# Performance work log

Measured on AMD Instinct MI355X. Metric: run time of the kernel, lower is better.

## Reference

```python
import jax, jax.numpy as jnp
import numpy as np
from jax import lax

# Dimensions (must match input_specs)
B, T, C = 2, 2048, 1024
H = 4 * C          # FFN hidden
E_RWKV, E_TRANS = 6, 2
E = E_RWKV + E_TRANS
LN_EPS = 1e-5


def layernorm(x, g, b):
    m = x.mean(-1, keepdims=True)
    v = ((x - m) ** 2).mean(-1, keepdims=True)
    return (x - m) * lax.rsqrt(v + LN_EPS) * g + b


def setup_inputs() -> dict:
    key = jax.random.key(0)
    ks = jax.random.split(key, 24)
    s = 0.02
    inp = {
        "x": jax.random.normal(ks[0], (B, T, C), jnp.float32),
        "v_first": jax.random.normal(ks[1], (B, T, C), jnp.float32),
        "winners": jax.random.randint(ks[2], (B, T, 2), 0, E),
        "capital_shares": jax.random.uniform(ks[3], (E,), jnp.float32),
        # LayerNorms
        "ln1_g": jnp.ones((C,), jnp.float32), "ln1_b": jnp.zeros((C,), jnp.float32),
        "ln2_g": jnp.ones((C,), jnp.float32), "ln2_b": jnp.zeros((C,), jnp.float32),
        # RWKV-style time-mix (simplified RWKV7_TimeMix)
        "Wr": s * jax.random.normal(ks[4], (C, C), jnp.float32),
        "Wk": s * jax.random.normal(ks[5], (C, C), jnp.float32),
        "Wv": s * jax.random.normal(ks[6], (C, C), jnp.float32),
        "Wo": s * jax.random.normal(ks[7], (C, C), jnp.float32),
        "w_decay": jax.random.normal(ks[8], (C,), jnp.float32),
        "g_v": jax.random.normal(ks[9], (C,), jnp.float32),
        # bridge: linear on concat(h, rwkv_state)
        "Wb": s * jax.random.normal(ks[10], (2 * C, C), jnp.float32),
        "bb": jnp.zeros((C,), jnp.float32),
        # 6 stacked SparseRWKVFFN experts: sigmoid(x Wr_r) * (relu(x Wk_r)^2 Wv_r)
        "Wk_r": s * jax.random.normal(ks[11], (E_RWKV, C, H), jnp.float32),
        "Wv_r": s * jax.random.normal(ks[12], (E_RWKV, H, C), jnp.float32),
        "Wr_r": s * jax.random.normal(ks[13], (E_RWKV, C, C), jnp.float32),
        # 2 stacked LinearTransformerExpert: gelu((h+prefix) W1) W2
        "W1_t": s * jax.random.normal(ks[14], (E_TRANS, C, H), jnp.float32),
        "W2_t": s * jax.random.normal(ks[15], (E_TRANS, H, C), jnp.float32),
    }
    return inp


def reference(x, v_first, winners, capital_shares,
              ln1_g, ln1_b, ln2_g, ln2_b,
              Wr, Wk, Wv, Wo, w_decay, g_v,
              Wb, bb, Wk_r, Wv_r, Wr_r, W1_t, W2_t):
    # ---- attention (simplified RWKV time-mix), returns per-token state ----
    h1 = layernorm(x, ln1_g, ln1_b)
    r = jax.nn.sigmoid(h1 @ Wr)                      # [B,T,C]
    k = h1 @ Wk
    v = h1 @ Wv
    v = v + (v_first - v) * jax.nn.sigmoid(g_v)      # value-residual mix
    w = jax.nn.sigmoid(w_decay)                      # per-channel decay [C]

    def step(s, kv):
        k_t, v_t = kv                                # [B,C] each
        s = w * s + k_t * v_t
        return s, s

    s0 = jnp.zeros((B, C), x.dtype)
    _, states = lax.scan(step, s0, (jnp.swapaxes(k, 0, 1), jnp.swapaxes(v, 0, 1)))
    states = jnp.swapaxes(states, 0, 1)              # rwkv_state [B,T,C]

    att_out = (r * states) @ Wo
    x = x + att_out
    h = layernorm(x, ln2_g, ln2_b)

    # ---- bridge prefix (flat over tokens, vectorized) ----
    bridge_prefix = jnp.concatenate([h, states], axis=-1) @ Wb + bb  # [B,T,C]

    # ---- experts computed densely, combined by top-2 gates ----
    # RWKV FFN experts
    a = jnp.square(jax.nn.relu(jnp.einsum('btc,ech->ebth', h, Wk_r)))     # [Er,B,T,H]
    rec = jax.nn.sigmoid(jnp.einsum('btc,ecd->ebtd', h, Wr_r))            # [Er,B,T,C]
    out_r = rec * jnp.einsum('ebth,ehc->ebtc', a, Wv_r)                   # [Er,B,T,C]
    # Linear-transformer experts consume the bridge prefix
    ht = h + bridge_prefix
    out_t = jnp.einsum('ebth,ehc->ebtc',
                       jax.nn.gelu(jnp.einsum('btc,ech->ebth', ht, W1_t)),
                       W2_t)                                              # [Et,B,T,C]
    all_out = jnp.concatenate([out_r, out_t], axis=0)                     # [E,B,T,C]

    # top-2 combine, each rank weighted 0.5 (use_market=False branch)
    gate = 0.5 * (jax.nn.one_hot(winners[..., 0], E, dtype=x.dtype)
                  + jax.nn.one_hot(winners[..., 1], E, dtype=x.dtype))    # [B,T,E]
    final_out = jnp.einsum('ebtc,bte->btc', all_out, gate)

    return x + final_out
```

## Files before the change

### kernel.cpp

```cpp
#include <hip/hip_runtime.h>

typedef unsigned short u16;
typedef __bf16 bf16x8 __attribute__((ext_vector_type(8)));
typedef float f32x4 __attribute__((ext_vector_type(4)));

__device__ __forceinline__ float bf2f(u16 u){ union{unsigned i;float f;}x; x.i=((unsigned)u)<<16; return x.f; }
__device__ __forceinline__ u16 f2bf(float f){ union{float f;unsigned i;}x; x.f=f; unsigned r = x.i + 0x7FFFu + ((x.i>>16)&1u); return (u16)(r>>16); }
__device__ __forceinline__ float sigm(float x){ return 1.f/(1.f+expf(-x)); }

struct __align__(8) U16x4 { u16 v[4]; };

__global__ void conv_t(const float* __restrict__ src, u16* __restrict__ dst, int K, int N){
  __shared__ u16 tile[64][72];
  const size_t mo = (size_t)blockIdx.z * (size_t)K * (size_t)N;
  src += mo; dst += mo;
  int k0 = blockIdx.x*64, n0 = blockIdx.y*64;
  int tid = threadIdx.x;
  #pragma unroll
  for (int it=0; it<4; ++it){
    int e = it*1024 + tid*4;
    int r = e>>6, c = e&63;
    float4 v = *(const float4*)(src + (size_t)(k0+r)*N + n0 + c);
    tile[r][c+0]=f2bf(v.x); tile[r][c+1]=f2bf(v.y); tile[r][c+2]=f2bf(v.z); tile[r][c+3]=f2bf(v.w);
  }
  __syncthreads();
  #pragma unroll
  for (int it=0; it<4; ++it){
    int e = it*1024 + tid*4;
    int n = e>>6, k = e&63;
    U16x4 o;
    #pragma unroll
    for (int j=0;j<4;++j) o.v[j] = tile[k+j][n];
    *(U16x4*)(dst + (size_t)(n0+n)*K + k0 + k) = o;
  }
}

__global__ void ln_k(const float* __restrict__ x, const float* __restrict__ g, const float* __restrict__ b,
                     u16* __restrict__ out, int ostride){
  int row = blockIdx.x, tid = threadIdx.x;
  float4 v = *(const float4*)(x + (size_t)row*1024 + tid*4);
  float s = v.x+v.y+v.z+v.w;
  float ss = v.x*v.x+v.y*v.y+v.z*v.z+v.w*v.w;
  #pragma unroll
  for (int o=32;o;o>>=1){ s += __shfl_down(s,o); ss += __shfl_down(ss,o); }
  __shared__ float sm[8];
  int lane = tid&63, wv = tid>>6;
  if (!lane){ sm[wv]=s; sm[4+wv]=ss; }
  __syncthreads();
  s = sm[0]+sm[1]+sm[2]+sm[3]; ss = sm[4]+sm[5]+sm[6]+sm[7];
  float mean = s*(1.f/1024.f);
  float var = ss*(1.f/1024.f) - mean*mean;
  float inv = rsqrtf(var + 1e-5f);
  U16x4 o;
  const float* vp = &v.x;
  #pragma unroll
  for (int j=0;j<4;++j){
    int c = tid*4+j;
    o.v[j] = f2bf((vp[j]-mean)*inv*g[c] + b[c]);
  }
  *(U16x4*)(out + (size_t)row*ostride + tid*4) = o;
}

__global__ void scan_p1(const u16* __restrict__ kbuf, const u16* __restrict__ vbuf,
                        const float* __restrict__ w_decay, float* __restrict__ carry){
  int c = blockIdx.x*256 + threadIdx.x;
  int chunk = blockIdx.y, b = blockIdx.z;
  float w = sigm(w_decay[c]);
  float s = 0.f;
  size_t idx = ((size_t)(b*2048 + chunk*64))*1024 + c;
  #pragma unroll 4
  for (int i=0;i<64;++i){ s = w*s + bf2f(kbuf[idx])*bf2f(vbuf[idx]); idx += 1024; }
  carry[((size_t)(b*32+chunk))*1024 + c] = s;
}
__global__ void scan_p2(const float* __restrict__ w_decay, const float* __restrict__ carry,
                        float* __restrict__ startv){
  int c = blockIdx.x*256 + threadIdx.x;
  int b = blockIdx.y;
  float w = sigm(w_decay[c]);
  float wL = w;
  #pragma unroll
  for (int i=0;i<6;++i) wL *= wL;
  float p = 0.f;
  for (int j=0;j<32;++j){
    size_t id = ((size_t)(b*32+j))*1024 + c;
    startv[id] = p;
    p = wL*p + carry[id];
  }
}
__global__ void scan_p3(const u16* __restrict__ kbuf, const u16* __restrict__ vbuf, const u16* __restrict__ rbuf,
                        const float* __restrict__ w_decay, const float* __restrict__ startv,
                        u16* __restrict__ rs, u16* __restrict__ hcat){
  int c = blockIdx.x*256 + threadIdx.x;
  int chunk = blockIdx.y, b = blockIdx.z;
  float w = sigm(w_decay[c]);
  float s = startv[((size_t)(b*32+chunk))*1024 + c];
  size_t t0 = (size_t)b*2048 + chunk*64;
  size_t idx = t0*1024 + c;
  size_t idx2 = t0*2048 + 1024 + c;
  for (int i=0;i<64;++i){
    s = w*s + bf2f(kbuf[idx])*bf2f(vbuf[idx]);
    rs[idx] = f2bf(bf2f(rbuf[idx]) * s);
    hcat[idx2] = f2bf(s);
    idx += 1024; idx2 += 2048;
  }
}

__global__ void route_count(const int* __restrict__ winners, int* __restrict__ offs, int* __restrict__ cursor){
  __shared__ int cnt[8];
  if (threadIdx.x < 8) cnt[threadIdx.x] = 0;
  __syncthreads();
  for (int p = threadIdx.x; p < 8192; p += 256) atomicAdd(&cnt[winners[p]&7], 1);
  __syncthreads();
  if (threadIdx.x == 0){
    int s = 0;
    #pragma unroll
    for (int e=0;e<8;++e){ offs[e]=s; s+=cnt[e]; }
    offs[8]=s;
  }
  if (threadIdx.x < 8) cursor[threadIdx.x] = 0;
}
__global__ void route_scatter(const int* __restrict__ winners, const int* __restrict__ offs,
                              int* __restrict__ cursor, int* __restrict__ idx_all){
  int p = blockIdx.x*256 + threadIdx.x;
  if (p < 8192){
    int e = winners[p]&7;
    int pos = offs[e] + atomicAdd(&cursor[e], 1);
    idx_all[pos] = p>>1;
  }
}

struct GArgs {
  const u16* A; const u16* B;
  long long lda, bstride;
  int K, N, Mdense, eBase;
  const int* offs; const int* idx_all;
  const float* x; const float* v_first; const float* g_v;
  u16* rbuf; u16* kbuf; u16* vbuf;
  float* out;
  const u16* hcat; const float* bb; u16* ht;
  u16* act; u16* rec;
};

template<int EPI, int GATHER>
__global__ __launch_bounds__(256,2) void gemm_k(GArgs g){
  int e = g.eBase + blockIdx.z;
  int rbase = 0, m = g.Mdense;
  if (g.offs){ rbase = g.offs[e]; m = g.offs[e+1] - rbase; }
  if ((int)blockIdx.y * 128 >= m) return;
  __shared__ char smem[32768];
  const int tid = threadIdx.x, lane = tid&63, wave = tid>>6;
  const int wr = wave>>1, wc = wave&1;

  int srow[4], scol[4];
  #pragma unroll
  for (int i=0;i<4;++i){
    srow[i] = i*32 + (tid>>3);
    scol[i] = ((((tid&7)*16) ^ ((srow[i]&7)<<4)) >> 1);
  }
  const u16* bBase[4];
  #pragma unroll
  for (int i=0;i<4;++i)
    bBase[i] = g.B + (long long)blockIdx.z*g.bstride
             + ((long long)blockIdx.x*128 + srow[i])*(long long)g.K + scol[i];

  int aOff[4][2], bOff[4][2];
  #pragma unroll
  for (int mm=0;mm<4;++mm){
    int rm = wr*64 + mm*16 + (lane&15);
    int rn = wc*64 + mm*16 + (lane&15);
    #pragma unroll
    for (int kk=0;kk<2;++kk){
      int X = kk*64 + (lane>>4)*16;
      aOff[mm][kk] = rm*128 + (X ^ ((rm&7)<<4));
      bOff[mm][kk] = 16384 + rn*128 + (X ^ ((rn&7)<<4));
    }
  }
  char* ldsA = smem + wave*1024;
  char* ldsB = smem + 16384 + wave*1024;
  const int nk = g.K >> 6;

  for (int mt = blockIdx.y; mt*128 < m; mt += gridDim.y){
    const u16* aSrc[4]; const u16* bSrc[4];
    #pragma unroll
    for (int i=0;i<4;++i){
      int grow = mt*128 + srow[i];
      int lr = grow < m ? grow : m-1;
      long long arow;
      if (GATHER) arow = g.idx_all[rbase + lr];
      else if (g.offs) arow = rbase + lr;
      else arow = grow;
      aSrc[i] = g.A + arow*g.lda + scol[i];
      bSrc[i] = bBase[i];
    }
    f32x4 acc[4][4];
    #pragma unroll
    for (int mm=0;mm<4;++mm)
      #pragma unroll
      for (int nn=0;nn<4;++nn)
        acc[mm][nn] = f32x4{0.f,0.f,0.f,0.f};

    for (int ks=0; ks<nk; ++ks){
      #pragma unroll
      for (int i=0;i<4;++i){
        __builtin_amdgcn_global_load_lds((const __attribute__((address_space(1))) void*)aSrc[i],
                                         (__attribute__((address_space(3))) void*)(ldsA + i*4096), 16, 0, 0);
        __builtin_amdgcn_global_load_lds((const __attribute__((address_space(1))) void*)bSrc[i],
                                         (__attribute__((address_space(3))) void*)(ldsB + i*4096), 16, 0, 0);
        aSrc[i] += 64; bSrc[i] += 64;
      }
      __syncthreads();
      #pragma unroll
      for (int kk=0;kk<2;++kk){
        bf16x8 af[4], bfv[4];
        #pragma unroll
        for (int q=0;q<4;++q) af[q] = *(const bf16x8*)(smem + aOff[q][kk]);
        #pragma unroll
        for (int q=0;q<4;++q) bfv[q] = *(const bf16x8*)(smem + bOff[q][kk]);
        #pragma unroll
        for (int mm=0;mm<4;++mm)
          #pragma unroll
          for (int nn=0;nn<4;++nn)
            acc[mm][nn] = __builtin_amdgcn_mfma_f32_16x16x32_bf16(af[mm], bfv[nn], acc[mm][nn], 0,0,0);
      }
      __syncthreads();
    }

    int colBase = blockIdx.x*128 + wc*64 + (lane&15);
    #pragma unroll
    for (int mm=0;mm<4;++mm){
      #pragma unroll
      for (int j=0;j<4;++j){
        int grow = mt*128 + wr*64 + mm*16 + (lane>>4)*4 + j;
        if (grow >= m) continue;
        size_t t = (size_t)grow;
        int gr = rbase + grow;
        #pragma unroll
        for (int nn=0;nn<4;++nn){
          int col = colBase + nn*16;
          float val = acc[mm][nn][j];
          if (EPI==0){
            if (col < 1024) g.rbuf[t*1024+col] = f2bf(sigm(val));
            else if (col < 2048) g.kbuf[t*1024+col-1024] = f2bf(val);
            else {
              int c2 = col-2048;
              float sg = sigm(g.g_v[c2]);
              float vf = g.v_first[t*1024+c2];
              g.vbuf[t*1024+c2] = f2bf(val + (vf-val)*sg);
            }
          } else if (EPI==1){
            g.out[t*1024+col] = g.x[t*1024+col] + val;
          } else if (EPI==2){
            g.ht[t*1024+col] = f2bf(bf2f(g.hcat[t*2048+col]) + val + g.bb[col]);
          } else if (EPI==3){
            float r_ = fmaxf(val, 0.f);
            g.act[(size_t)gr*4096+col] = f2bf(r_*r_);
          } else if (EPI==4){
            g.rec[(size_t)gr*1024+col] = f2bf(sigm(val));
          } else if (EPI==5){
            int tok = g.idx_all[gr];
            float rc = bf2f(g.rec[(size_t)gr*1024+col]);
            atomicAdd(&g.out[(size_t)tok*1024+col], 0.5f*val*rc);
          } else if (EPI==6){
            float t3 = val*val*val;
            float th = tanhf(0.79788456080286535588f*(val + 0.044715f*t3));
            g.act[(size_t)gr*4096+col] = f2bf(0.5f*val*(1.f+th));
          } else if (EPI==7){
            int tok = g.idx_all[gr];
            atomicAdd(&g.out[(size_t)tok*1024+col], 0.5f*val);
          }
        }
      }
    }
  }
}

extern "C" void kernel_launch(void* const* d_in, const int* in_sizes, int n_in,
                              void* d_out, int out_size, void* d_ws, size_t ws_size,
                              hipStream_t stream) {
  const float* x       = (const float*)d_in[0];
  const float* v_first = (const float*)d_in[1];
  const int*   winners = (const int*)d_in[2];
  const float* ln1_g   = (const float*)d_in[4];
  const float* ln1_b   = (const float*)d_in[5];
  const float* ln2_g   = (const float*)d_in[6];
  const float* ln2_b   = (const float*)d_in[7];
  const float* Wr      = (const float*)d_in[8];
  const float* Wk      = (const float*)d_in[9];
  const float* Wv      = (const float*)d_in[10];
  const float* Wo      = (const float*)d_in[11];
  const float* w_decay = (const float*)d_in[12];
  const float* g_v     = (const float*)d_in[13];
  const float* Wb      = (const float*)d_in[14];
  const float* bb      = (const float*)d_in[15];
  const float* Wk_r    = (const float*)d_in[16];
  const float* Wv_r    = (const float*)d_in[17];
  const float* Wr_r    = (const float*)d_in[18];
  const float* W1_t    = (const float*)d_in[19];
  const float* W2_t    = (const float*)d_in[20];
  float* out = (float*)d_out;

  char* p = (char*)d_ws;
  auto alloc = [&](size_t bytes)->char*{ char* r=p; p += (bytes+255)&~(size_t)255; return r; };
  u16* wTrkv = (u16*)alloc(3072ull*1024*2);
  u16* wTo   = (u16*)alloc(1024ull*1024*2);
  u16* wTb   = (u16*)alloc(1024ull*2048*2);
  u16* wTkr  = (u16*)alloc(6ull*4096*1024*2);
  u16* wTvr  = (u16*)alloc(6ull*1024*4096*2);
  u16* wTrr  = (u16*)alloc(6ull*1024*1024*2);
  u16* wT1   = (u16*)alloc(2ull*4096*1024*2);
  u16* wT2   = (u16*)alloc(2ull*1024*4096*2);
  u16* h1    = (u16*)alloc(4096ull*1024*2);
  u16* rbuf  = (u16*)alloc(4096ull*1024*2);
  u16* kbuf  = (u16*)alloc(4096ull*1024*2);
  u16* vbuf  = (u16*)alloc(4096ull*1024*2);
  u16* rsb   = (u16*)alloc(4096ull*1024*2);
  u16* hcat  = (u16*)alloc(4096ull*2048*2);
  u16* htb   = (u16*)alloc(4096ull*1024*2);
  u16* act   = (u16*)alloc(8192ull*4096*2);
  u16* rec   = (u16*)alloc(8192ull*1024*2);
  float* carry  = (float*)alloc(2ull*32*1024*4);
  float* startv = (float*)alloc(2ull*32*1024*4);
  int* offs   = (int*)alloc(16*4);
  int* cursor = (int*)alloc(8*4);
  int* idx_all= (int*)alloc(8192*4);

  dim3 B256(256);

  conv_t<<<dim3(16,16,1),B256,0,stream>>>(Wr,   wTrkv,            1024,1024);
  conv_t<<<dim3(16,16,1),B256,0,stream>>>(Wk,   wTrkv+1024*1024,  1024,1024);
  conv_t<<<dim3(16,16,1),B256,0,stream>>>(Wv,   wTrkv+2048*1024,  1024,1024);
  conv_t<<<dim3(16,16,1),B256,0,stream>>>(Wo,   wTo,              1024,1024);
  conv_t<<<dim3(32,16,1),B256,0,stream>>>(Wb,   wTb,              2048,1024);
  conv_t<<<dim3(16,64,6),B256,0,stream>>>(Wk_r, wTkr,             1024,4096);
  conv_t<<<dim3(64,16,6),B256,0,stream>>>(Wv_r, wTvr,             4096,1024);
  conv_t<<<dim3(16,16,6),B256,0,stream>>>(Wr_r, wTrr,             1024,1024);
  conv_t<<<dim3(16,64,2),B256,0,stream>>>(W1_t, wT1,              1024,4096);
  conv_t<<<dim3(64,16,2),B256,0,stream>>>(W2_t, wT2,              4096,1024);

  route_count<<<1,B256,0,stream>>>(winners, offs, cursor);
  route_scatter<<<32,B256,0,stream>>>(winners, offs, cursor, idx_all);

  ln_k<<<4096,B256,0,stream>>>(x, ln1_g, ln1_b, h1, 1024);

  {
    GArgs ga{}; ga.A=h1; ga.B=wTrkv; ga.lda=1024; ga.bstride=0; ga.K=1024; ga.N=3072; ga.Mdense=4096;
    ga.v_first=v_first; ga.g_v=g_v; ga.rbuf=rbuf; ga.kbuf=kbuf; ga.vbuf=vbuf;
    gemm_k<0,0><<<dim3(24,32,1),B256,0,stream>>>(ga);
  }

  scan_p1<<<dim3(4,32,2),B256,0,stream>>>(kbuf, vbuf, w_decay, carry);
  scan_p2<<<dim3(4,2,1), B256,0,stream>>>(w_decay, carry, startv);
  scan_p3<<<dim3(4,32,2),B256,0,stream>>>(kbuf, vbuf, rbuf, w_decay, startv, rsb, hcat);

  {
    GArgs ga{}; ga.A=rsb; ga.B=wTo; ga.lda=1024; ga.K=1024; ga.N=1024; ga.Mdense=4096;
    ga.x=x; ga.out=out;
    gemm_k<1,0><<<dim3(8,32,1),B256,0,stream>>>(ga);
  }

  ln_k<<<4096,B256,0,stream>>>(out, ln2_g, ln2_b, hcat, 2048);

  {
    GArgs ga{}; ga.A=hcat; ga.B=wTb; ga.lda=2048; ga.K=2048; ga.N=1024; ga.Mdense=4096;
    ga.hcat=hcat; ga.bb=bb; ga.ht=htb;
    gemm_k<2,0><<<dim3(8,32,1),B256,0,stream>>>(ga);
  }

  {
    GArgs ga{}; ga.A=hcat; ga.B=wTkr; ga.lda=2048; ga.bstride=4096ll*1024; ga.K=1024; ga.N=4096;
    ga.offs=offs; ga.eBase=0; ga.idx_all=idx_all; ga.act=act;
    gemm_k<3,1><<<dim3(32,12,6),B256,0,stream>>>(ga);
  }
  {
    GArgs ga{}; ga.A=hcat; ga.B=wTrr; ga.lda=2048; ga.bstride=1024ll*1024; ga.K=1024; ga.N=1024;
    ga.offs=offs; ga.eBase=0; ga.idx_all=idx_all; ga.rec=rec;
    gemm_k<4,1><<<dim3(8,12,6),B256,0,stream>>>(ga);
  }
  {
    GArgs ga{}; ga.A=act; ga.B=wTvr; ga.lda=4096; ga.bstride=1024ll*4096; ga.K=4096; ga.N=1024;
    ga.offs=offs; ga.eBase=0; ga.idx_all=idx_all; ga.rec=rec; ga.out=out;
    gemm_k<5,0><<<dim3(8,12,6),B256,0,stream>>>(ga);
  }
  {
    GArgs ga{}; ga.A=htb; ga.B=wT1; ga.lda=1024; ga.bstride=4096ll*1024; ga.K=1024; ga.N=4096;
    ga.offs=offs; ga.eBase=6; ga.idx_all=idx_all; ga.act=act;
    gemm_k<6,1><<<dim3(32,12,2),B256,0,stream>>>(ga);
  }
  {
    GArgs ga{}; ga.A=act; ga.B=wT2; ga.lda=4096; ga.bstride=1024ll*4096; ga.K=4096; ga.N=1024;
    ga.offs=offs; ga.eBase=6; ga.idx_all=idx_all; ga.out=out;
    gemm_k<7,0><<<dim3(8,12,2),B256,0,stream>>>(ga);
  }

  (void)in_sizes; (void)n_in; (void)out_size; (void)ws_size;
}
```

Measured before the change: 800.6 us.

## Double-buffer LDS tiles in GEMM mainloop with async global-to-LDS prefetch

Doubles the shared memory to two 32KB stages and prefetches the next K-slice directly into LDS while MFMAs consume the current one. Explicit vmcnt and lgkmcnt waits plus raw barriers replace __syncthreads. This hides global load latency behind compute. With 64KB LDS per block, fewer blocks may fit per CU than the two requested by launch bounds, so occupancy may drop.

```diff
diff --git a/kernel.cpp b/kernel.cpp
--- a/kernel.cpp
+++ b/kernel.cpp
@@ -141,13 +141,16 @@
   u16* act; u16* rec;
 };
 
+#define GLL(gp, lp) __builtin_amdgcn_global_load_lds((const __attribute__((address_space(1))) void*)(gp), \
+                                                     (__attribute__((address_space(3))) void*)(lp), 16, 0, 0)
+
 template<int EPI, int GATHER>
 __global__ __launch_bounds__(256,2) void gemm_k(GArgs g){
   int e = g.eBase + blockIdx.z;
   int rbase = 0, m = g.Mdense;
   if (g.offs){ rbase = g.offs[e]; m = g.offs[e+1] - rbase; }
   if ((int)blockIdx.y * 128 >= m) return;
-  __shared__ char smem[32768];
+  __shared__ char smem[65536];
   const int tid = threadIdx.x, lane = tid&63, wave = tid>>6;
   const int wr = wave>>1, wc = wave&1;
 
@@ -199,30 +202,44 @@
       for (int nn=0;nn<4;++nn)
         acc[mm][nn] = f32x4{0.f,0.f,0.f,0.f};
 
+    #pragma unroll
+    for (int i=0;i<4;++i){
+      GLL(aSrc[i], ldsA + i*4096);
+      GLL(bSrc[i], ldsB + i*4096);
+      aSrc[i] += 64; bSrc[i] += 64;
+    }
+    int cur = 0;
     for (int ks=0; ks<nk; ++ks){
-      #pragma unroll
-      for (int i=0;i<4;++i){
-        __builtin_amdgcn_global_load_lds((const __attribute__((address_space(1))) void*)aSrc[i],
-                                         (__attribute__((address_space(3))) void*)(ldsA + i*4096), 16, 0, 0);
-        __builtin_amdgcn_global_load_lds((const __attribute__((address_space(1))) void*)bSrc[i],
-                                         (__attribute__((address_space(3))) void*)(ldsB + i*4096), 16, 0, 0);
-        aSrc[i] += 64; bSrc[i] += 64;
+      if (ks+1 < nk){
+        int nb = (cur^1)*32768;
+        #pragma unroll
+        for (int i=0;i<4;++i){
+          GLL(aSrc[i], ldsA + nb + i*4096);
+          GLL(bSrc[i], ldsB + nb + i*4096);
+          aSrc[i] += 64; bSrc[i] += 64;
+        }
+        asm volatile("s_waitcnt vmcnt(8)" ::: "memory");
+      } else {
+        asm volatile("s_waitcnt vmcnt(0)" ::: "memory");
       }
-      __syncthreads();
+      asm volatile("s_barrier" ::: "memory");
+      const char* base = smem + cur*32768;
       #pragma unroll
       for (int kk=0;kk<2;++kk){
         bf16x8 af[4], bfv[4];
         #pragma unroll
-        for (int q=0;q<4;++q) af[q] = *(const bf16x8*)(smem + aOff[q][kk]);
+        for (int q=0;q<4;++q) af[q] = *(const bf16x8*)(base + aOff[q][kk]);
         #pragma unroll
-        for (int q=0;q<4;++q) bfv[q] = *(const bf16x8*)(smem + bOff[q][kk]);
+        for (int q=0;q<4;++q) bfv[q] = *(const bf16x8*)(base + bOff[q][kk]);
         #pragma unroll
         for (int mm=0;mm<4;++mm)
           #pragma unroll
           for (int nn=0;nn<4;++nn)
             acc[mm][nn] = __builtin_amdgcn_mfma_f32_16x16x32_bf16(af[mm], bfv[nn], acc[mm][nn], 0,0,0);
       }
-      __syncthreads();
+      asm volatile("s_waitcnt lgkmcnt(0)" ::: "memory");
+      asm volatile("s_barrier" ::: "memory");
+      cur ^= 1;
     }
 
     int colBase = blockIdx.x*128 + wc*64 + (lane&15);
```

Result: faster. 753.7 us (-5.9%).
